# Kernel tuning notes

Hardware: AMD Instinct MI355X
Metric: run time of the kernel (lower is better)

## Reference

```python
import jax, jax.numpy as jnp
import numpy as np

N_NODES = 100000
N_EDGES = 1600000
IN_CH = 128
HID = 64
BN_EPS = 1e-5


def setup_inputs() -> dict:
    key = jax.random.key(0)
    ks = jax.random.split(key, 16)
    x = jax.random.normal(ks[0], (N_NODES, IN_CH), dtype=jnp.float32)
    edge_index = jax.random.randint(ks[1], (2, N_EDGES), 0, N_NODES, dtype=jnp.int32)
    edge_weight = jax.random.uniform(ks[2], (N_EDGES,), dtype=jnp.float32)
    # GCNConv layer params (weight [in, out], bias [out])
    W1 = jax.random.normal(ks[3], (IN_CH, HID), dtype=jnp.float32) / np.sqrt(IN_CH)
    b1 = jnp.zeros((HID,), jnp.float32)
    W2 = jax.random.normal(ks[4], (HID, HID), dtype=jnp.float32) / np.sqrt(HID)
    b2 = jnp.zeros((HID,), jnp.float32)
    # BatchNorm affine params
    g1 = jnp.ones((HID,), jnp.float32)
    beta1 = jnp.zeros((HID,), jnp.float32)
    g2 = jnp.ones((HID,), jnp.float32)
    beta2 = jnp.zeros((HID,), jnp.float32)
    # input projection for residual (in_channels != hidden_dim)
    pW = jax.random.normal(ks[5], (IN_CH, HID), dtype=jnp.float32) / np.sqrt(IN_CH)
    pb = jnp.zeros((HID,), jnp.float32)
    return {"x": x, "edge_index": edge_index, "edge_weight": edge_weight,
            "W1": W1, "b1": b1, "g1": g1, "beta1": beta1,
            "W2": W2, "b2": b2, "g2": g2, "beta2": beta2,
            "pW": pW, "pb": pb}


def _gcn_norm(edge_index, edge_weight, num_nodes):
    # add self-loops with weight 1, symmetric normalization (PyG gcn_norm)
    loop = jnp.arange(num_nodes, dtype=edge_index.dtype)
    row = jnp.concatenate([edge_index[0], loop])   # source
    col = jnp.concatenate([edge_index[1], loop])   # target
    w = jnp.concatenate([edge_weight, jnp.ones((num_nodes,), edge_weight.dtype)])
    deg = jax.ops.segment_sum(w, col, num_segments=num_nodes)  # weighted in-degree
    dis = jnp.where(deg > 0, jax.lax.rsqrt(jnp.where(deg > 0, deg, 1.0)), 0.0)
    norm = dis[row] * w * dis[col]  # [E+N]
    return row, col, norm


def _conv(h, W, b, row, col, norm, num_nodes):
    hw = h @ W                                      # [N, out]
    msg = hw[row] * norm[:, None]                   # gather + scale, [E+N, out]
    return jax.ops.segment_sum(msg, col, num_segments=num_nodes) + b


def _bn(h, g, beta):
    mu = jnp.mean(h, axis=0)
    var = jnp.var(h, axis=0)
    return g * (h - mu) * jax.lax.rsqrt(var + BN_EPS) + beta


def reference(x, edge_index, edge_weight, W1, b1, g1, beta1, W2, b2, g2, beta2, pW, pb):
    n = x.shape[0]
    row, col, norm = _gcn_norm(edge_index, edge_weight, n)
    residual = x @ pW + pb                          # input_proj residual
    # layer 1: conv -> BN -> ReLU -> (dropout=identity) -> + residual
    h = jax.nn.relu(_bn(_conv(x, W1, b1, row, col, norm, n), g1, beta1)) + residual
    # layer 2: conv -> BN -> ReLU -> + h_in
    h_in = h
    h = jax.nn.relu(_bn(_conv(h, W2, b2, row, col, norm, n), g2, beta2)) + h_in
    return h
```

## Files before the change

kernel.cpp:

```cpp
#include <hip/hip_runtime.h>

static constexpr float BN_EPS = 1e-5f;
typedef unsigned int uint;
typedef unsigned short ushort;

__device__ __forceinline__ void fatomic_add(float* p, float v) {
  unsafeAtomicAdd(p, v);
}

__device__ __forceinline__ ushort f2bf(float f) {
  uint u = __float_as_uint(f);
  u += 0x7fffu + ((u >> 16) & 1u);
  return (ushort)(u >> 16);
}

__device__ __forceinline__ float4 bf4_decode(uint2 r) {
  return make_float4(__uint_as_float(r.x << 16), __uint_as_float(r.x & 0xffff0000u),
                     __uint_as_float(r.y << 16), __uint_as_float(r.y & 0xffff0000u));
}

__global__ void k_hist(const int* __restrict__ col, int* __restrict__ cnt,
                       int* __restrict__ rank, int e) {
  int i = blockIdx.x * 256 + threadIdx.x;
  if (i < e) rank[i] = atomicAdd(&cnt[col[i]], 1);
}

__global__ __launch_bounds__(256) void k_scan_part(const int* __restrict__ cnt,
                                                   int* __restrict__ bsum, int n) {
  __shared__ int sm[256];
  int t = threadIdx.x;
  int base = blockIdx.x * 1024 + t * 4;
  int s = 0;
#pragma unroll
  for (int j = 0; j < 4; j++) {
    int i = base + j;
    if (i < n) s += cnt[i];
  }
  sm[t] = s;
  __syncthreads();
  for (int off = 128; off > 0; off >>= 1) {
    if (t < off) sm[t] += sm[t + off];
    __syncthreads();
  }
  if (t == 0) bsum[blockIdx.x] = sm[0];
}

__global__ __launch_bounds__(1024) void k_scan_mid(int* __restrict__ bsum, int nb) {
  __shared__ int sm[1024];
  int t = threadIdx.x;
  int v = (t < nb) ? bsum[t] : 0;
  sm[t] = v;
  __syncthreads();
  for (int off = 1; off < 1024; off <<= 1) {
    int o = (t >= off) ? sm[t - off] : 0;
    __syncthreads();
    sm[t] += o;
    __syncthreads();
  }
  if (t < nb) bsum[t] = sm[t] - v;
}

__global__ __launch_bounds__(256) void k_scan_apply(const int* __restrict__ cnt,
                                                    int* __restrict__ ptr,
                                                    const int* __restrict__ bsum,
                                                    int n, int e) {
  __shared__ int sm[256];
  int t = threadIdx.x;
  int base = blockIdx.x * 1024 + t * 4;
  int v[4];
  int s = 0;
#pragma unroll
  for (int j = 0; j < 4; j++) {
    int i = base + j;
    v[j] = (i < n) ? cnt[i] : 0;
    s += v[j];
  }
  sm[t] = s;
  __syncthreads();
  for (int off = 1; off < 256; off <<= 1) {
    int o = (t >= off) ? sm[t - off] : 0;
    __syncthreads();
    sm[t] += o;
    __syncthreads();
  }
  int run = bsum[blockIdx.x] + sm[t] - s;
#pragma unroll
  for (int j = 0; j < 4; j++) {
    int i = base + j;
    if (i < n) {
      ptr[i] = run;
      run += v[j];
    }
  }
  if (blockIdx.x == 0 && t == 0) ptr[n] = e;
}

__global__ void k_fillcsr(const int* __restrict__ row, const int* __restrict__ col,
                          const float* __restrict__ ew, const int* __restrict__ ptr,
                          const int* __restrict__ rank, int2* __restrict__ spair, int e) {
  int i = blockIdx.x * 256 + threadIdx.x;
  if (i >= e) return;
  int p = ptr[col[i]] + rank[i];
  spair[p] = make_int2(row[i], __float_as_int(ew[i]));
}

__global__ void k_degdis(const int* __restrict__ ptr, const int2* __restrict__ spair,
                         float* __restrict__ dis, int n) {
  int v = blockIdx.x * 256 + threadIdx.x;
  if (v >= n) return;
  int b = ptr[v], en = ptr[v + 1];
  float s = 1.0f;
  for (int j = b; j < en; j++) s += __int_as_float(spair[j].y);
  dis[v] = rsqrtf(s);
}

__global__ void k_scale(int2* __restrict__ spair, const float* __restrict__ dis, int e) {
  int i = blockIdx.x * 256 + threadIdx.x;
  if (i >= e) return;
  int2 m = spair[i];
  spair[i] = make_int2(m.x, __float_as_int(__int_as_float(m.y) * dis[m.x]));
}

__global__ __launch_bounds__(256) void k_agg(
    const int* __restrict__ ptr, const int2* __restrict__ spair,
    const float* __restrict__ dis, const ushort* __restrict__ hwb,
    float* __restrict__ agg, float* __restrict__ stats, int n) {
  int lane = threadIdx.x & 63;
  int grp = lane >> 4;
  int li = lane & 15;
  int wid = blockIdx.x * 4 + (threadIdx.x >> 6);
  int nw = gridDim.x * 4;
  float st_s[4] = {0.f, 0.f, 0.f, 0.f};
  float st_q[4] = {0.f, 0.f, 0.f, 0.f};

  for (int vb = wid * 4; vb < n; vb += nw * 4) {
    int v = vb + grp;
    bool on = v < n;
    float4 acc = make_float4(0.f, 0.f, 0.f, 0.f);
    float d = 0.f;
    int beg = 0, end = 0;
    if (on) {
      beg = ptr[v];
      end = ptr[v + 1];
      d = dis[v];
      uint2 rs = *(const uint2*)(hwb + (size_t)v * 64 + li * 4);
      float4 f = bf4_decode(rs);
      acc = make_float4(d * f.x, d * f.y, d * f.z, d * f.w);
    }
    if (on && beg < end) {
      const int4* sp = (const int4*)spair;
      int jc = beg & ~3;
      int h = jc >> 1;
      int nch = (end - jc + 3) >> 2;
      int4 a0 = sp[h], a1 = sp[h + 1];
      int4 b0, b1;
      if (nch > 1) { b0 = sp[h + 2]; b1 = sp[h + 3]; }
      float wC[4];
      uint2 gC[4];
      {
        int rr[4] = {a0.x, a0.z, a1.x, a1.z};
        int wi[4] = {a0.y, a0.w, a1.y, a1.w};
#pragma unroll
        for (int k = 0; k < 4; k++) {
          int idx = jc + k;
          bool okk = (idx >= beg) && (idx < end);
          int r = okk ? rr[k] : v;
          wC[k] = okk ? __int_as_float(wi[k]) : 0.f;
          gC[k] = *(const uint2*)(hwb + (size_t)r * 64 + li * 4);
        }
      }
      for (int c = 0; c < nch; c++) {
        float wN[4];
        uint2 gN[4];
        if (c + 1 < nch) {
          int jn = jc + 4;
          int rr[4] = {b0.x, b0.z, b1.x, b1.z};
          int wi[4] = {b0.y, b0.w, b1.y, b1.w};
#pragma unroll
          for (int k = 0; k < 4; k++) {
            bool okk = (jn + k) < end;
            int r = okk ? rr[k] : v;
            wN[k] = okk ? __int_as_float(wi[k]) : 0.f;
            gN[k] = *(const uint2*)(hwb + (size_t)r * 64 + li * 4);
          }
        }
        if (c + 2 < nch) {
          b0 = sp[h + 2 * (c + 2)];
          b1 = sp[h + 2 * (c + 2) + 1];
        }
#pragma unroll
        for (int k = 0; k < 4; k++) {
          float4 f = bf4_decode(gC[k]);
          acc.x = fmaf(wC[k], f.x, acc.x);
          acc.y = fmaf(wC[k], f.y, acc.y);
          acc.z = fmaf(wC[k], f.z, acc.z);
          acc.w = fmaf(wC[k], f.w, acc.w);
        }
        if (c + 1 < nch) {
#pragma unroll
          for (int k = 0; k < 4; k++) { gC[k] = gN[k]; wC[k] = wN[k]; }
        }
        jc += 4;
      }
    }
    if (on) {
      acc.x *= d; acc.y *= d; acc.z *= d; acc.w *= d;
      *(float4*)(agg + (size_t)v * 64 + li * 4) = acc;
      st_s[0] += acc.x; st_s[1] += acc.y; st_s[2] += acc.z; st_s[3] += acc.w;
      st_q[0] = fmaf(acc.x, acc.x, st_q[0]);
      st_q[1] = fmaf(acc.y, acc.y, st_q[1]);
      st_q[2] = fmaf(acc.z, acc.z, st_q[2]);
      st_q[3] = fmaf(acc.w, acc.w, st_q[3]);
    }
  }

#pragma unroll
  for (int j = 0; j < 4; j++) {
    st_s[j] += __shfl_xor(st_s[j], 16);
    st_s[j] += __shfl_xor(st_s[j], 32);
    st_q[j] += __shfl_xor(st_q[j], 16);
    st_q[j] += __shfl_xor(st_q[j], 32);
  }
  __shared__ float rs[4][64];
  __shared__ float rq[4][64];
  int wv = threadIdx.x >> 6;
  if (grp == 0) {
#pragma unroll
    for (int j = 0; j < 4; j++) {
      rs[wv][li * 4 + j] = st_s[j];
      rq[wv][li * 4 + j] = st_q[j];
    }
  }
  __syncthreads();
  if (threadIdx.x < 64) {
    int c = threadIdx.x;
    float s = rs[0][c] + rs[1][c] + rs[2][c] + rs[3][c];
    float q = rq[0][c] + rq[1][c] + rq[2][c] + rq[3][c];
    fatomic_add(&stats[c], s);
    fatomic_add(&stats[64 + c], q);
  }
}

template <int K, int N, int KT, bool SPLIT>
__global__ __launch_bounds__(256) void k_gemmv(
    const float* __restrict__ x, const float* __restrict__ Wa,
    const float* __restrict__ Wb, const float* __restrict__ bb,
    ushort* __restrict__ ob, float* __restrict__ of, int n) {
  constexpr int CS = N / 16;
  constexpr int RS = 256 / CS;
  constexpr int TR = RS * 4;
  __shared__ float wS[KT * N];
  int tid = threadIdx.x;
  int cseg = tid % CS;
  int rslot = tid / CS;
  int baseRow = blockIdx.x * TR;

  float acc[4][16];
#pragma unroll
  for (int i = 0; i < 4; i++)
#pragma unroll
    for (int j = 0; j < 16; j++) acc[i][j] = 0.f;

  int rows[4];
  bool ok[4];
#pragma unroll
  for (int i = 0; i < 4; i++) {
    rows[i] = baseRow + rslot + i * RS;
    ok[i] = rows[i] < n;
  }

  for (int kt = 0; kt < K; kt += KT) {
    __syncthreads();
    for (int idx = tid; idx < KT * N / 4; idx += 256) {
      int kk = idx / (N / 4);
      int c4 = idx % (N / 4);
      const float* src = (SPLIT && c4 >= 16) ? Wb : Wa;
      int cc = SPLIT ? (c4 & 15) : c4;
      ((float4*)wS)[idx] = ((const float4*)(src + (size_t)(kt + kk) * 64))[cc];
    }
    __syncthreads();
#pragma unroll 2
    for (int k4 = 0; k4 < KT / 4; k4++) {
      float4 xv[4];
#pragma unroll
      for (int i = 0; i < 4; i++)
        xv[i] = ok[i] ? *(const float4*)(x + (size_t)rows[i] * K + kt + k4 * 4)
                      : make_float4(0.f, 0.f, 0.f, 0.f);
#pragma unroll
      for (int u = 0; u < 4; u++) {
        const float4* wr = (const float4*)(wS + (k4 * 4 + u) * N + cseg * 16);
        float4 w0 = wr[0], w1 = wr[1], w2 = wr[2], w3 = wr[3];
#pragma unroll
        for (int i = 0; i < 4; i++) {
          float ak = (u == 0) ? xv[i].x : (u == 1) ? xv[i].y : (u == 2) ? xv[i].z : xv[i].w;
          acc[i][0] = fmaf(ak, w0.x, acc[i][0]);
          acc[i][1] = fmaf(ak, w0.y, acc[i][1]);
          acc[i][2] = fmaf(ak, w0.z, acc[i][2]);
          acc[i][3] = fmaf(ak, w0.w, acc[i][3]);
          acc[i][4] = fmaf(ak, w1.x, acc[i][4]);
          acc[i][5] = fmaf(ak, w1.y, acc[i][5]);
          acc[i][6] = fmaf(ak, w1.z, acc[i][6]);
          acc[i][7] = fmaf(ak, w1.w, acc[i][7]);
          acc[i][8] = fmaf(ak, w2.x, acc[i][8]);
          acc[i][9] = fmaf(ak, w2.y, acc[i][9]);
          acc[i][10] = fmaf(ak, w2.z, acc[i][10]);
          acc[i][11] = fmaf(ak, w2.w, acc[i][11]);
          acc[i][12] = fmaf(ak, w3.x, acc[i][12]);
          acc[i][13] = fmaf(ak, w3.y, acc[i][13]);
          acc[i][14] = fmaf(ak, w3.z, acc[i][14]);
          acc[i][15] = fmaf(ak, w3.w, acc[i][15]);
        }
      }
    }
  }

  if (!SPLIT || cseg < CS / 2) {
    int co = cseg * 16;
#pragma unroll
    for (int i = 0; i < 4; i++) {
      if (!ok[i]) continue;
      ushort* o = ob + (size_t)rows[i] * 64 + co;
      uint pk[8];
#pragma unroll
      for (int q = 0; q < 8; q++)
        pk[q] = (uint)f2bf(acc[i][2 * q]) | ((uint)f2bf(acc[i][2 * q + 1]) << 16);
      ((uint4*)o)[0] = make_uint4(pk[0], pk[1], pk[2], pk[3]);
      ((uint4*)o)[1] = make_uint4(pk[4], pk[5], pk[6], pk[7]);
    }
  } else {
    int cs = cseg - CS / 2;
    float4 bv[4];
#pragma unroll
    for (int q = 0; q < 4; q++) bv[q] = ((const float4*)bb)[cs * 4 + q];
#pragma unroll
    for (int i = 0; i < 4; i++) {
      if (!ok[i]) continue;
      float* o = of + (size_t)rows[i] * 64 + cs * 16;
#pragma unroll
      for (int q = 0; q < 4; q++)
        ((float4*)o)[q] = make_float4(acc[i][q * 4 + 0] + bv[q].x, acc[i][q * 4 + 1] + bv[q].y,
                                      acc[i][q * 4 + 2] + bv[q].z, acc[i][q * 4 + 3] + bv[q].w);
    }
  }
}

__global__ __launch_bounds__(256) void k_bnrelu(
    const float* __restrict__ agg, const float* __restrict__ res,
    const float* __restrict__ stats, const float* __restrict__ g,
    const float* __restrict__ beta, float* __restrict__ out, int n) {
  int idx = blockIdx.x * 256 + threadIdx.x;
  if (idx >= n * 16) return;
  int c4 = (idx & 15) * 4;
  float invN = 1.0f / (float)n;
  float4 a = ((const float4*)agg)[idx];
  float4 rr = ((const float4*)res)[idx];
  float av[4] = {a.x, a.y, a.z, a.w};
  float rv[4] = {rr.x, rr.y, rr.z, rr.w};
  float vo[4];
#pragma unroll
  for (int j = 0; j < 4; j++) {
    int c = c4 + j;
    float mu = stats[c] * invN;
    float var = stats[64 + c] * invN - mu * mu;
    float sc = g[c] * rsqrtf(var + BN_EPS);
    float v = (av[j] - mu) * sc + beta[c];
    vo[j] = fmaxf(v, 0.0f) + rv[j];
  }
  ((float4*)out)[idx] = make_float4(vo[0], vo[1], vo[2], vo[3]);
}

extern "C" void kernel_launch(void* const* d_in, const int* in_sizes, int n_in,
                              void* d_out, int out_size, void* d_ws, size_t ws_size,
                              hipStream_t stream) {
  const float* x = (const float*)d_in[0];
  const int* ei = (const int*)d_in[1];
  const float* ew = (const float*)d_in[2];
  const float* W1 = (const float*)d_in[3];
  const float* g1 = (const float*)d_in[5];
  const float* be1 = (const float*)d_in[6];
  const float* W2 = (const float*)d_in[7];
  const float* g2 = (const float*)d_in[9];
  const float* be2 = (const float*)d_in[10];
  const float* pW = (const float*)d_in[11];
  const float* pb = (const float*)d_in[12];

  int n = in_sizes[0] / 128;
  int e = in_sizes[1] / 2;
  const int* row = ei;
  const int* col = ei + e;

  float* ws = (float*)d_ws;
  float* dis = ws;
  int* ptr = (int*)(dis + n);
  int* cnt = ptr + n + 4;
  int* rank = cnt + n;
  int* bsum = rank + e;
  int2* spair = (int2*)(bsum + 1024);
  ushort* hwb = (ushort*)(spair + e + 16);
  float* bufR = (float*)(hwb + (size_t)n * 64);
  float* bufB = bufR + (size_t)n * 64;
  float* bufA = bufB + (size_t)n * 64;
  float* stats = bufA + (size_t)n * 64;

  float* out = (float*)d_out;

  int nb_n = (n + 255) / 256;
  int nb_e = (e + 255) / 256;
  int nb_b = (n * 16 + 255) / 256;
  int nb_sc = (n + 1023) / 1024;
  int nb_g1 = (n + 127) / 128;
  int nb_g2 = (n + 255) / 256;

  hipMemsetAsync(cnt, 0, n * sizeof(int), stream);
  k_hist<<<nb_e, 256, 0, stream>>>(col, cnt, rank, e);
  k_scan_part<<<nb_sc, 256, 0, stream>>>(cnt, bsum, n);
  k_scan_mid<<<1, 1024, 0, stream>>>(bsum, nb_sc);
  k_scan_apply<<<nb_sc, 256, 0, stream>>>(cnt, ptr, bsum, n, e);
  k_fillcsr<<<nb_e, 256, 0, stream>>>(row, col, ew, ptr, rank, spair, e);
  k_degdis<<<nb_n, 256, 0, stream>>>(ptr, spair, dis, n);
  k_scale<<<nb_e, 256, 0, stream>>>(spair, dis, e);

  k_gemmv<128, 128, 64, true><<<nb_g1, 256, 0, stream>>>(x, W1, pW, pb, hwb, bufR, n);
  hipMemsetAsync(stats, 0, 128 * sizeof(float), stream);
  k_agg<<<2048, 256, 0, stream>>>(ptr, spair, dis, hwb, bufB, stats, n);
  k_bnrelu<<<nb_b, 256, 0, stream>>>(bufB, bufR, stats, g1, be1, bufA, n);

  k_gemmv<64, 64, 64, false><<<nb_g2, 256, 0, stream>>>(bufA, W2, nullptr, nullptr, hwb, nullptr, n);
  hipMemsetAsync(stats, 0, 128 * sizeof(float), stream);
  k_agg<<<2048, 256, 0, stream>>>(ptr, spair, dis, hwb, bufB, stats, n);
  k_bnrelu<<<nb_b, 256, 0, stream>>>(bufB, bufA, stats, g2, be2, out, n);
}
```

Baseline: 476.0 us.

## Replace FP32 FMA GEMMs with bf16 MFMA kernels using swizzled LDS weights

Both dense projections (x@[W1|pW] and h@W2) are rewritten to use 16x16x32 bf16 MFMA instructions instead of scalar FP32 FMAs. Weights are transposed into LDS as bf16 with an XOR swizzle to avoid bank conflicts, and activations are converted to bf16 in registers. This aims to cut GEMM compute time, but it lowers precision of the residual projection output, which was previously exact fp32, and writes outputs with narrow scattered stores.

Result: faster. 416.6 us (-12.5%).

```diff
diff --git a/kernel.cpp b/kernel.cpp
--- a/kernel.cpp
+++ b/kernel.cpp
@@ -3,6 +3,8 @@
 static constexpr float BN_EPS = 1e-5f;
 typedef unsigned int uint;
 typedef unsigned short ushort;
+typedef __attribute__((ext_vector_type(8))) short bf16x8;
+typedef __attribute__((ext_vector_type(4))) float f32x4;
 
 __device__ __forceinline__ void fatomic_add(float* p, float v) {
   unsafeAtomicAdd(p, v);
@@ -241,105 +243,165 @@
   }
 }
 
-template <int K, int N, int KT, bool SPLIT>
-__global__ __launch_bounds__(256) void k_gemmv(
-    const float* __restrict__ x, const float* __restrict__ Wa,
-    const float* __restrict__ Wb, const float* __restrict__ bb,
+__global__ __launch_bounds__(256) void k_gemm1m(
+    const float* __restrict__ x, const float* __restrict__ W1,
+    const float* __restrict__ pW, const float* __restrict__ pb,
     ushort* __restrict__ ob, float* __restrict__ of, int n) {
-  constexpr int CS = N / 16;
-  constexpr int RS = 256 / CS;
-  constexpr int TR = RS * 4;
-  __shared__ float wS[KT * N];
+  __shared__ ushort wT[128 * 128];
   int tid = threadIdx.x;
-  int cseg = tid % CS;
-  int rslot = tid / CS;
-  int baseRow = blockIdx.x * TR;
-
-  float acc[4][16];
-#pragma unroll
-  for (int i = 0; i < 4; i++)
-#pragma unroll
-    for (int j = 0; j < 16; j++) acc[i][j] = 0.f;
-
-  int rows[4];
-  bool ok[4];
-#pragma unroll
-  for (int i = 0; i < 4; i++) {
-    rows[i] = baseRow + rslot + i * RS;
-    ok[i] = rows[i] < n;
-  }
-
-  for (int kt = 0; kt < K; kt += KT) {
-    __syncthreads();
-    for (int idx = tid; idx < KT * N / 4; idx += 256) {
-      int kk = idx / (N / 4);
-      int c4 = idx % (N / 4);
-      const float* src = (SPLIT && c4 >= 16) ? Wb : Wa;
-      int cc = SPLIT ? (c4 & 15) : c4;
-      ((float4*)wS)[idx] = ((const float4*)(src + (size_t)(kt + kk) * 64))[cc];
-    }
-    __syncthreads();
-#pragma unroll 2
-    for (int k4 = 0; k4 < KT / 4; k4++) {
-      float4 xv[4];
-#pragma unroll
-      for (int i = 0; i < 4; i++)
-        xv[i] = ok[i] ? *(const float4*)(x + (size_t)rows[i] * K + kt + k4 * 4)
-                      : make_float4(0.f, 0.f, 0.f, 0.f);
-#pragma unroll
-      for (int u = 0; u < 4; u++) {
-        const float4* wr = (const float4*)(wS + (k4 * 4 + u) * N + cseg * 16);
-        float4 w0 = wr[0], w1 = wr[1], w2 = wr[2], w3 = wr[3];
-#pragma unroll
-        for (int i = 0; i < 4; i++) {
-          float ak = (u == 0) ? xv[i].x : (u == 1) ? xv[i].y : (u == 2) ? xv[i].z : xv[i].w;
-          acc[i][0] = fmaf(ak, w0.x, acc[i][0]);
-          acc[i][1] = fmaf(ak, w0.y, acc[i][1]);
-          acc[i][2] = fmaf(ak, w0.z, acc[i][2]);
-          acc[i][3] = fmaf(ak, w0.w, acc[i][3]);
-          acc[i][4] = fmaf(ak, w1.x, acc[i][4]);
-          acc[i][5] = fmaf(ak, w1.y, acc[i][5]);
-          acc[i][6] = fmaf(ak, w1.z, acc[i][6]);
-          acc[i][7] = fmaf(ak, w1.w, acc[i][7]);
-          acc[i][8] = fmaf(ak, w2.x, acc[i][8]);
-          acc[i][9] = fmaf(ak, w2.y, acc[i][9]);
-          acc[i][10] = fmaf(ak, w2.z, acc[i][10]);
-          acc[i][11] = fmaf(ak, w2.w, acc[i][11]);
-          acc[i][12] = fmaf(ak, w3.x, acc[i][12]);
-          acc[i][13] = fmaf(ak, w3.y, acc[i][13]);
-          acc[i][14] = fmaf(ak, w3.z, acc[i][14]);
-          acc[i][15] = fmaf(ak, w3.w, acc[i][15]);
-        }
-      }
-    }
-  }
-
-  if (!SPLIT || cseg < CS / 2) {
-    int co = cseg * 16;
-#pragma unroll
-    for (int i = 0; i < 4; i++) {
-      if (!ok[i]) continue;
-      ushort* o = ob + (size_t)rows[i] * 64 + co;
-      uint pk[8];
-#pragma unroll
-      for (int q = 0; q < 8; q++)
-        pk[q] = (uint)f2bf(acc[i][2 * q]) | ((uint)f2bf(acc[i][2 * q + 1]) << 16);
-      ((uint4*)o)[0] = make_uint4(pk[0], pk[1], pk[2], pk[3]);
-      ((uint4*)o)[1] = make_uint4(pk[4], pk[5], pk[6], pk[7]);
-    }
-  } else {
-    int cs = cseg - CS / 2;
-    float4 bv[4];
-#pragma unroll
-    for (int q = 0; q < 4; q++) bv[q] = ((const float4*)bb)[cs * 4 + q];
-#pragma unroll
-    for (int i = 0; i < 4; i++) {
-      if (!ok[i]) continue;
-      float* o = of + (size_t)rows[i] * 64 + cs * 16;
-#pragma unroll
-      for (int q = 0; q < 4; q++)
-        ((float4*)o)[q] = make_float4(acc[i][q * 4 + 0] + bv[q].x, acc[i][q * 4 + 1] + bv[q].y,
-                                      acc[i][q * 4 + 2] + bv[q].z, acc[i][q * 4 + 3] + bv[q].w);
+  for (int idx = tid; idx < 128 * 64; idx += 256) {
+    int c = idx >> 6;
+    int kp = idx & 63;
+    const float* src = (c < 64) ? (W1 + c) : (pW + (c - 64));
+    float f0 = src[(size_t)(2 * kp) * 64];
+    float f1 = src[(size_t)(2 * kp + 1) * 64];
+    uint pk = (uint)f2bf(f0) | ((uint)f2bf(f1) << 16);
+    int byte = c * 256 + kp * 4;
+    byte ^= ((c & 7) << 4);
+    *(uint*)((char*)wT + byte) = pk;
+  }
+  __syncthreads();
+
+  int lane = tid & 63;
+  int wv = tid >> 6;
+  int lr = lane & 15;
+  int lk = lane >> 4;
+  int rowBase = blockIdx.x * 128 + wv * 32;
+
+  f32x4 acc[2][8];
+#pragma unroll
+  for (int i = 0; i < 2; i++)
+#pragma unroll
+    for (int j = 0; j < 8; j++) acc[i][j] = (f32x4){0.f, 0.f, 0.f, 0.f};
+
+  int r0 = rowBase + lr;
+  int r1 = rowBase + 16 + lr;
+  bool ok0 = r0 < n, ok1 = r1 < n;
+  int swz = (lr & 7) << 4;
+
+#pragma unroll
+  for (int ks = 0; ks < 4; ks++) {
+    int k0 = ks * 32 + lk * 8;
+    bf16x8 a0 = (bf16x8)(short)0, a1 = (bf16x8)(short)0;
+    if (ok0) {
+      const float4* xp = (const float4*)(x + (size_t)r0 * 128 + k0);
+      float4 v0 = xp[0], v1 = xp[1];
+      a0[0] = (short)f2bf(v0.x); a0[1] = (short)f2bf(v0.y);
+      a0[2] = (short)f2bf(v0.z); a0[3] = (short)f2bf(v0.w);
+      a0[4] = (short)f2bf(v1.x); a0[5] = (short)f2bf(v1.y);
+      a0[6] = (short)f2bf(v1.z); a0[7] = (short)f2bf(v1.w);
+    }
+    if (ok1) {
+      const float4* xp = (const float4*)(x + (size_t)r1 * 128 + k0);
+      float4 v0 = xp[0], v1 = xp[1];
+      a1[0] = (short)f2bf(v0.x); a1[1] = (short)f2bf(v0.y);
+      a1[2] = (short)f2bf(v0.z); a1[3] = (short)f2bf(v0.w);
+      a1[4] = (short)f2bf(v1.x); a1[5] = (short)f2bf(v1.y);
+      a1[6] = (short)f2bf(v1.z); a1[7] = (short)f2bf(v1.w);
+    }
+#pragma unroll
+    for (int ct = 0; ct < 8; ct++) {
+      int byte = ((ct * 16 + lr) * 128 + k0) * 2;
+      byte ^= swz;
+      bf16x8 b = *(const bf16x8*)((const char*)wT + byte);
+      acc[0][ct] = __builtin_amdgcn_mfma_f32_16x16x32_bf16(a0, b, acc[0][ct], 0, 0, 0);
+      acc[1][ct] = __builtin_amdgcn_mfma_f32_16x16x32_bf16(a1, b, acc[1][ct], 0, 0, 0);
+    }
+  }
+
+  float bias[4];
+#pragma unroll
+  for (int q = 0; q < 4; q++) bias[q] = pb[q * 16 + lr];
+
+#pragma unroll
+  for (int rt = 0; rt < 2; rt++) {
+#pragma unroll
+    for (int e = 0; e < 4; e++) {
+      int r = rowBase + rt * 16 + lk * 4 + e;
+      if (r >= n) continue;
+#pragma unroll
+      for (int ct = 0; ct < 4; ct++)
+        ob[(size_t)r * 64 + ct * 16 + lr] = f2bf(acc[rt][ct][e]);
+#pragma unroll
+      for (int ct = 4; ct < 8; ct++)
+        of[(size_t)r * 64 + (ct - 4) * 16 + lr] = acc[rt][ct][e] + bias[ct - 4];
+    }
+  }
+}
+
+__global__ __launch_bounds__(256) void k_gemm2m(
+    const float* __restrict__ h, const float* __restrict__ W2,
+    ushort* __restrict__ ob, int n) {
+  __shared__ ushort wT[64 * 64];
+  int tid = threadIdx.x;
+  for (int idx = tid; idx < 64 * 32; idx += 256) {
+    int c = idx >> 5;
+    int kp = idx & 31;
+    float f0 = W2[(size_t)(2 * kp) * 64 + c];
+    float f1 = W2[(size_t)(2 * kp + 1) * 64 + c];
+    uint pk = (uint)f2bf(f0) | ((uint)f2bf(f1) << 16);
+    int byte = c * 128 + kp * 4;
+    byte ^= ((c & 7) << 4);
+    *(uint*)((char*)wT + byte) = pk;
+  }
+  __syncthreads();
+
+  int lane = tid & 63;
+  int wv = tid >> 6;
+  int lr = lane & 15;
+  int lk = lane >> 4;
+  int rowBase = blockIdx.x * 128 + wv * 32;
+
+  f32x4 acc[2][4];
+#pragma unroll
+  for (int i = 0; i < 2; i++)
+#pragma unroll
+    for (int j = 0; j < 4; j++) acc[i][j] = (f32x4){0.f, 0.f, 0.f, 0.f};
+
+  int r0 = rowBase + lr;
+  int r1 = rowBase + 16 + lr;
+  bool ok0 = r0 < n, ok1 = r1 < n;
+  int swz = (lr & 7) << 4;
+
+#pragma unroll
+  for (int ks = 0; ks < 2; ks++) {
+    int k0 = ks * 32 + lk * 8;
+    bf16x8 a0 = (bf16x8)(short)0, a1 = (bf16x8)(short)0;
+    if (ok0) {
+      const float4* xp = (const float4*)(h + (size_t)r0 * 64 + k0);
+      float4 v0 = xp[0], v1 = xp[1];
+      a0[0] = (short)f2bf(v0.x); a0[1] = (short)f2bf(v0.y);
+      a0[2] = (short)f2bf(v0.z); a0[3] = (short)f2bf(v0.w);
+      a0[4] = (short)f2bf(v1.x); a0[5] = (short)f2bf(v1.y);
+      a0[6] = (short)f2bf(v1.z); a0[7] = (short)f2bf(v1.w);
+    }
+    if (ok1) {
+      const float4* xp = (const float4*)(h + (size_t)r1 * 64 + k0);
+      float4 v0 = xp[0], v1 = xp[1];
+      a1[0] = (short)f2bf(v0.x); a1[1] = (short)f2bf(v0.y);
+      a1[2] = (short)f2bf(v0.z); a1[3] = (short)f2bf(v0.w);
+      a1[4] = (short)f2bf(v1.x); a1[5] = (short)f2bf(v1.y);
+      a1[6] = (short)f2bf(v1.z); a1[7] = (short)f2bf(v1.w);
+    }
+#pragma unroll
+    for (int ct = 0; ct < 4; ct++) {
+      int byte = ((ct * 16 + lr) * 64 + k0) * 2;
+      byte ^= swz;
+      bf16x8 b = *(const bf16x8*)((const char*)wT + byte);
+      acc[0][ct] = __builtin_amdgcn_mfma_f32_16x16x32_bf16(a0, b, acc[0][ct], 0, 0, 0);
+      acc[1][ct] = __builtin_amdgcn_mfma_f32_16x16x32_bf16(a1, b, acc[1][ct], 0, 0, 0);
+    }
+  }
+
+#pragma unroll
+  for (int rt = 0; rt < 2; rt++) {
+#pragma unroll
+    for (int e = 0; e < 4; e++) {
+      int r = rowBase + rt * 16 + lk * 4 + e;
+      if (r >= n) continue;
+#pragma unroll
+      for (int ct = 0; ct < 4; ct++)
+        ob[(size_t)r * 64 + ct * 16 + lr] = f2bf(acc[rt][ct][e]);
     }
   }
 }
@@ -408,8 +470,7 @@
   int nb_e = (e + 255) / 256;
   int nb_b = (n * 16 + 255) / 256;
   int nb_sc = (n + 1023) / 1024;
-  int nb_g1 = (n + 127) / 128;
-  int nb_g2 = (n + 255) / 256;
+  int nb_g = (n + 127) / 128;
 
   hipMemsetAsync(cnt, 0, n * sizeof(int), stream);
   k_hist<<<nb_e, 256, 0, stream>>>(col, cnt, rank, e);
@@ -420,12 +481,12 @@
   k_degdis<<<nb_n, 256, 0, stream>>>(ptr, spair, dis, n);
   k_scale<<<nb_e, 256, 0, stream>>>(spair, dis, e);
 
-  k_gemmv<128, 128, 64, true><<<nb_g1, 256, 0, stream>>>(x, W1, pW, pb, hwb, bufR, n);
+  k_gemm1m<<<nb_g, 256, 0, stream>>>(x, W1, pW, pb, hwb, bufR, n);
   hipMemsetAsync(stats, 0, 128 * sizeof(float), stream);
   k_agg<<<2048, 256, 0, stream>>>(ptr, spair, dis, hwb, bufB, stats, n);
   k_bnrelu<<<nb_b, 256, 0, stream>>>(bufB, bufR, stats, g1, be1, bufA, n);
 
-  k_gemmv<64, 64, 64, false><<<nb_g2, 256, 0, stream>>>(bufA, W2, nullptr, nullptr, hwb, nullptr, n);
+  k_gemm2m<<<nb_g, 256, 0, stream>>>(bufA, W2, hwb, n);
   hipMemsetAsync(stats, 0, 128 * sizeof(float), stream);
   k_agg<<<2048, 256, 0, stream>>>(ptr, spair, dis, hwb, bufB, stats, n);
   k_bnrelu<<<nb_b, 256, 0, stream>>>(bufB, bufA, stats, g2, be2, out, n);
```
